# Kernel tuning notes

Measured on AMD Instinct MI355X. Metric: run time of the kernel, lower is better.

## Reference

```python
import jax, jax.numpy as jnp
import numpy as np

NEG_POS_RATIO = 3
BETA = 1.0
ALPHA = 2.0


def _smooth_ex_loss(pred, tgt):
    # a = beta / (1 - exp(-alpha)); c = a - beta - beta/alpha
    a = BETA / (1.0 - np.exp(-ALPHA))
    c = a - BETA - BETA / ALPHA
    diff = jnp.abs(pred - tgt)
    return jnp.where(diff < 1.0,
                     a * (diff + (jnp.exp(-ALPHA * diff) - 1.0) / ALPHA),
                     BETA * diff + c)


def setup_inputs() -> dict:
    key = jax.random.key(0)
    k1, k2, k3, k4 = jax.random.split(key, 4)
    B, P, C = 128, 8732, 21
    return {
        "confidence": jax.random.normal(k1, (B, P, C), dtype=jnp.float32),
        "predicted_locations": jax.random.normal(k2, (B, P, 4), dtype=jnp.float32),
        "labels": jax.random.randint(k3, (B, P), 0, C, dtype=jnp.int64),
        "gt_locations": jax.random.normal(k4, (B, P, 4), dtype=jnp.float32),
    }


def reference(confidence, predicted_locations, labels, gt_locations):
    # confidence: [B, P, C]; labels: [B, P]; locations: [B, P, 4]
    logp = jax.nn.log_softmax(confidence, axis=2)
    pos_mask = labels > 0

    # --- hard negative mining (no-grad in original) ---
    bg_loss = jax.lax.stop_gradient(-logp[:, :, 0])          # [B, P]
    num_pos = pos_mask.sum(axis=1, keepdims=True)             # [B, 1]
    num_neg = num_pos * NEG_POS_RATIO
    mined = jnp.where(pos_mask, -jnp.inf, bg_loss)
    idx = jnp.argsort(-mined, axis=1)                         # descending sort
    orders = jnp.argsort(idx, axis=1)                         # rank of each prior
    neg_mask = orders < num_neg
    mask = pos_mask | neg_mask                                # [B, P]

    # --- classification loss: sum of CE over mined priors ---
    per_elem_ce = -jnp.take_along_axis(logp, labels[..., None], axis=2)[..., 0]
    classification_loss = jnp.sum(jnp.where(mask, per_elem_ce, 0.0))

    # --- localization loss: smooth-ex loss over positive priors ---
    loc = _smooth_ex_loss(predicted_locations, gt_locations)  # [B, P, 4]
    smooth_sum = jnp.sum(jnp.where(pos_mask[..., None], loc, 0.0))

    n_pos_total = pos_mask.sum().astype(jnp.float32)
    return (smooth_sum / n_pos_total, classification_loss / n_pos_total)
```

## Files before the change

### kernel.cpp

```cpp
#include <hip/hip_runtime.h>
#include <cstdint>


#define B_ 128
#define P_ 8732
#define C_ 21
constexpr int TPB = 128;
constexpr int SPR = 28;
constexpr int SPAN = 312;
constexpr int NCHK = 5;
constexpr int GRID = B_ * SPR / 2;
constexpr int SLOTS = SPR / 2;
constexpr int CHB = 64 * C_ * 4;

typedef const __attribute__((address_space(1))) uint32_t* gas_u32p;
typedef __attribute__((address_space(3))) uint32_t* las_u32p;

__device__ __forceinline__ float waveSumF(float v) {
#pragma unroll
  for (int o = 32; o; o >>= 1) v += __shfl_down(v, o);
  return v;
}
__device__ __forceinline__ int waveSumI(int v) {
#pragma unroll
  for (int o = 32; o; o >>= 1) v += __shfl_down(v, o);
  return v;
}
__device__ __forceinline__ double waveSumD(double v) {
#pragma unroll
  for (int o = 32; o; o >>= 1) v += __shfl_down(v, o);
  return v;
}

__device__ __forceinline__ void stage(const char* g, float* l, int bytes, int lane) {
#pragma unroll
  for (int j = 0; j < 6; ++j) {
    const int off = (j << 10) + (lane << 4);
    if (off < bytes)
      __builtin_amdgcn_global_load_lds((gas_u32p)(g + off),
                                       (las_u32p)(l + (j << 8)), 16, 0, 0);
  }
}

#define SMEX(d) (((d) < 1.f) ? (1.1565176427496657f * ((d) + (__expf(-2.f * (d)) - 1.f) * 0.5f)) \
                             : ((d) - 0.3434823572503343f))

__device__ __forceinline__ void prior21(const float* lp, int lab, float4 pr, float4 gv,
                                        bool act, float& sm, float& cp, float& cn, int& np) {
  const float f0 = lp[0], f1 = lp[1], f2 = lp[2], f3 = lp[3], f4 = lp[4];
  const float f5 = lp[5], f6 = lp[6], f7 = lp[7], f8 = lp[8], f9 = lp[9];
  const float f10 = lp[10], f11 = lp[11], f12 = lp[12], f13 = lp[13], f14 = lp[14];
  const float f15 = lp[15], f16 = lp[16], f17 = lp[17], f18 = lp[18], f19 = lp[19];
  const float f20 = lp[20];
  float m = fmaxf(fmaxf(fmaxf(fmaxf(f0, f1), fmaxf(f2, f3)),
                        fmaxf(fmaxf(f4, f5), fmaxf(f6, f7))),
                  fmaxf(fmaxf(fmaxf(f8, f9), fmaxf(f10, f11)),
                        fmaxf(fmaxf(f12, f13), fmaxf(f14, f15))));
  m = fmaxf(m, fmaxf(fmaxf(fmaxf(f16, f17), fmaxf(f18, f19)), f20));
  float s = __expf(f0 - m) + __expf(f1 - m) + __expf(f2 - m) + __expf(f3 - m);
  s += __expf(f4 - m) + __expf(f5 - m) + __expf(f6 - m) + __expf(f7 - m);
  s += __expf(f8 - m) + __expf(f9 - m) + __expf(f10 - m) + __expf(f11 - m);
  s += __expf(f12 - m) + __expf(f13 - m) + __expf(f14 - m) + __expf(f15 - m);
  s += __expf(f16 - m) + __expf(f17 - m) + __expf(f18 - m) + __expf(f19 - m);
  s += __expf(f20 - m);
  float xl = f0;
  xl = (lab == 1) ? f1 : xl;   xl = (lab == 2) ? f2 : xl;
  xl = (lab == 3) ? f3 : xl;   xl = (lab == 4) ? f4 : xl;
  xl = (lab == 5) ? f5 : xl;   xl = (lab == 6) ? f6 : xl;
  xl = (lab == 7) ? f7 : xl;   xl = (lab == 8) ? f8 : xl;
  xl = (lab == 9) ? f9 : xl;   xl = (lab == 10) ? f10 : xl;
  xl = (lab == 11) ? f11 : xl; xl = (lab == 12) ? f12 : xl;
  xl = (lab == 13) ? f13 : xl; xl = (lab == 14) ? f14 : xl;
  xl = (lab == 15) ? f15 : xl; xl = (lab == 16) ? f16 : xl;
  xl = (lab == 17) ? f17 : xl; xl = (lab == 18) ? f18 : xl;
  xl = (lab == 19) ? f19 : xl; xl = (lab == 20) ? f20 : xl;
  const float ce = m + __logf(s) - xl;

  float d, smx;
  d = fabsf(pr.x - gv.x); smx = SMEX(d);
  d = fabsf(pr.y - gv.y); smx += SMEX(d);
  d = fabsf(pr.z - gv.z); smx += SMEX(d);
  d = fabsf(pr.w - gv.w); smx += SMEX(d);

  const bool pos = act && (lab > 0);
  sm += pos ? smx : 0.f;
  cp += pos ? ce : 0.f;
  cn += (act && lab == 0) ? ce : 0.f;
  np += pos ? 1 : 0;
}

__global__ __launch_bounds__(TPB, 3) void k_main(
    const float* __restrict__ conf, const float* __restrict__ pred,
    const int* __restrict__ labels, const float* __restrict__ gt,
    float4* __restrict__ part) {
  __shared__ __align__(16) float sbuf[2][2][64 * C_];
  __shared__ float redf[6];
  __shared__ int redi[2];
  const int tid = threadIdx.x;
  const int wid = tid >> 6, lane = tid & 63;
  const int row = blockIdx.x / SLOTS;
  const int pair = blockIdx.x % SLOTS;
  const int s = pair * 2 + wid;
  const int ps = s * SPAN;
  const int spc = min(SPAN, P_ - ps);
  const size_t rp = (size_t)row * P_;
  const char* cbase = (const char*)conf + (rp + (size_t)ps) * (C_ * 4);
  const float4* pred4 = (const float4*)pred;
  const float4* gt4 = (const float4*)gt;
  float* wbuf0 = sbuf[wid][0];
  float* wbuf1 = sbuf[wid][1];

  stage(cbase, wbuf0, 64 * C_ * 4, lane);
  int labr;
  float4 prr, gvr;
  {
    const size_t gp = rp + ps + lane;
    labr = labels[gp];
    prr = pred4[gp];
    gvr = gt4[gp];
  }
  asm volatile("s_waitcnt vmcnt(0)" ::: "memory");
  __builtin_amdgcn_sched_barrier(0);

  float sm = 0.f, cp = 0.f, cn = 0.f;
  int np = 0;

#pragma unroll
  for (int k = 0; k < NCHK; ++k) {
    float* cbuf = (k & 1) ? wbuf1 : wbuf0;
    float* nbuf = (k & 1) ? wbuf0 : wbuf1;
    int labn = 0;
    float4 prn = make_float4(0, 0, 0, 0), gvn = prn;
    if (k + 1 < NCHK) {
      const int cntn = min(64, spc - ((k + 1) << 6));
      stage(cbase + (size_t)(k + 1) * CHB, nbuf, cntn * (C_ * 4), lane);
      int idx = ((k + 1) << 6) + lane;
      if (idx >= spc) idx = spc - 1;
      const size_t gp = rp + ps + idx;
      labn = labels[gp];
      prn = pred4[gp];
      gvn = gt4[gp];
    }

    const int cnt = min(64, spc - (k << 6));
    prior21(&cbuf[lane * C_], labr, prr, gvr, lane < cnt, sm, cp, cn, np);

    asm volatile("s_waitcnt vmcnt(0)" ::: "memory");
    __builtin_amdgcn_sched_barrier(0);
    labr = labn; prr = prn; gvr = gvn;
  }

  const float r0 = waveSumF(sm), r1 = waveSumF(cp), r2 = waveSumF(cn);
  const int r3 = waveSumI(np);
  if (lane == 0) { redf[wid] = r0; redf[2 + wid] = r1; redf[4 + wid] = r2; redi[wid] = r3; }
  __syncthreads();
  if (tid == 0) {
    part[blockIdx.x] = make_float4(redf[0] + redf[1], redf[2] + redf[3],
                                   redf[4] + redf[5], (float)(redi[0] + redi[1]));
  }
}

__device__ __forceinline__ unsigned keyCE(const float* __restrict__ conf,
                                          const int* __restrict__ labels,
                                          int b, int p, float& ce) {
  const float* row = conf + ((size_t)b * P_ + p) * C_;
  float m = row[0];
  for (int c = 1; c < C_; ++c) m = fmaxf(m, row[c]);
  float s = 0.f;
  for (int c = 0; c < C_; ++c) s += __expf(row[c] - m);
  const float lse = m + __logf(s);
  const int lab = labels[(size_t)b * P_ + p];
  ce = lse - row[lab];
  if (lab > 0) return 0u;
  unsigned u = __float_as_uint(lse - row[0]);
  u = (u & 0x80000000u) ? ~u : (u | 0x80000000u);
  return u ? u : 1u;
}

__global__ __launch_bounds__(128) void k_tail(
    const float4* __restrict__ part, const float* __restrict__ conf,
    const int* __restrict__ labels, float* __restrict__ out) {
  const int tid = threadIdx.x;
  const int wid = tid >> 6, lane = tid & 63;
  __shared__ int s_np[B_], s_flag[B_];
  __shared__ double sdA[2], sdB[2], sdC[2];
  __shared__ int siN[2];
  __shared__ double s_extra;
  __shared__ int icnt[2];
  __shared__ float fsum[2];

  double sm = 0.0, cp = 0.0, cnSel = 0.0;
  int npr = 0;
  {
    double cn = 0.0;
#pragma unroll
    for (int i = 0; i < SLOTS; ++i) {
      const float4 v = part[tid * SLOTS + i];
      sm += (double)v.x;
      cp += (double)v.y;
      cn += (double)v.z;
      npr += (int)v.w;
    }
    s_np[tid] = npr;
    const int fl = (3 * npr < P_ - npr) ? 1 : 0;
    s_flag[tid] = fl;
    if (!fl) cnSel = cn;
  }
  const double t1 = waveSumD(sm), t2 = waveSumD(cp), t3 = waveSumD(cnSel);
  const int t4 = waveSumI(npr);
  if (lane == 0) { sdA[wid] = t1; sdB[wid] = t2; sdC[wid] = t3; siN[wid] = t4; }
  if (tid == 0) s_extra = 0.0;
  __syncthreads();

  for (int b = 0; b < B_; ++b) {
    if (!s_flag[b]) continue;
    const int need = 3 * s_np[b];
    unsigned long long lo = 1, hi = 0xFFFFFFFFull, ans = 1;
    while (lo <= hi) {
      const unsigned long long mid = lo + ((hi - lo) >> 1);
      int c = 0;
      float dummy;
      for (int p = tid; p < P_; p += 128)
        if ((unsigned long long)keyCE(conf, labels, b, p, dummy) >= mid) c++;
      c = waveSumI(c);
      if (lane == 0) icnt[wid] = c;
      __syncthreads();
      const int tot = icnt[0] + icnt[1];
      if (tot >= need) { ans = mid; lo = mid + 1; } else { hi = mid - 1; }
      __syncthreads();
    }
    int cgt = 0;
    float sgt = 0.f;
    for (int p = tid; p < P_; p += 128) {
      float ce;
      const unsigned long long k = keyCE(conf, labels, b, p, ce);
      if (k > ans) { cgt++; sgt += ce; }
    }
    cgt = waveSumI(cgt);
    sgt = waveSumF(sgt);
    if (lane == 0) { icnt[wid] = cgt; fsum[wid] = sgt; }
    __syncthreads();
    if (tid == 0) {
      const int gtot = icnt[0] + icnt[1];
      double sx = (double)(fsum[0] + fsum[1]);
      int rm = need - gtot;
      int taken = 0;
      for (int p = 0; p < P_ && taken < rm; ++p) {
        float ce;
        if (keyCE(conf, labels, b, p, ce) == ans) { sx += ce; taken++; }
      }
      s_extra += sx;
    }
    __syncthreads();
  }

  if (tid == 0) {
    const double G0 = sdA[0] + sdA[1];
    const double G1 = sdB[0] + sdB[1];
    const double G2 = sdC[0] + sdC[1] + s_extra;
    const double N = (double)(siN[0] + siN[1]);
    out[0] = (float)(G0 / N);
    out[1] = (float)((G1 + G2) / N);
  }
}

extern "C" void kernel_launch(void* const* d_in, const int* in_sizes, int n_in,
                              void* d_out, int out_size, void* d_ws, size_t ws_size,
                              hipStream_t stream) {
  const float* conf = (const float*)d_in[0];
  const float* pred = (const float*)d_in[1];
  const int* labels = (const int*)d_in[2];
  const float* gt = (const float*)d_in[3];
  float* out = (float*)d_out;

  float4* part = (float4*)d_ws;

  hipLaunchKernelGGL(k_main, dim3(GRID), dim3(TPB), 0, stream,
                     conf, pred, labels, gt, part);
  hipLaunchKernelGGL(k_tail, dim3(1), dim3(128), 0, stream,
                     part, conf, labels, out);
}
```

Baseline: 41.98 us.

## Use single-wave blocks with triple-buffered LDS ring and deeper prefetch

Replaces the two-wave blocks, each with its own double buffer, by one-wave blocks that own a 640-prior span and stream it through a three-slot LDS ring. Up to two chunks stay in flight, with partial vmcnt waits and per-chunk bounds clamping in place of byte-count guards. Block-level shared reduction is dropped because each block writes its partial directly. The goal is to hide global-load latency better and cut sync overhead, at the cost of fewer, longer-lived blocks and more LDS per wave.

```diff
diff --git a/kernel.cpp b/kernel.cpp
--- a/kernel.cpp
+++ b/kernel.cpp
@@ -5,13 +5,14 @@
 #define B_ 128
 #define P_ 8732
 #define C_ 21
-constexpr int TPB = 128;
-constexpr int SPR = 28;
-constexpr int SPAN = 312;
-constexpr int NCHK = 5;
-constexpr int GRID = B_ * SPR / 2;
-constexpr int SLOTS = SPR / 2;
+constexpr int TPB = 64;
+constexpr int SPR = 14;
+constexpr int SPAN = 640;
+constexpr int NCHK = 10;
+constexpr int GRID = B_ * SPR;
 constexpr int CHB = 64 * C_ * 4;
+constexpr int BUFF = 1536;
+constexpr size_t NE = (size_t)B_ * P_;
 
 typedef const __attribute__((address_space(1))) uint32_t* gas_u32p;
 typedef __attribute__((address_space(3))) uint32_t* las_u32p;
@@ -32,13 +33,13 @@
   return v;
 }
 
-__device__ __forceinline__ void stage(const char* g, float* l, int bytes, int lane) {
+__device__ __forceinline__ void stage6(const char* g, const char* gend,
+                                       float* l, int lane) {
 #pragma unroll
   for (int j = 0; j < 6; ++j) {
-    const int off = (j << 10) + (lane << 4);
-    if (off < bytes)
-      __builtin_amdgcn_global_load_lds((gas_u32p)(g + off),
-                                       (las_u32p)(l + (j << 8)), 16, 0, 0);
+    const char* s = g + (j << 10) + (lane << 4);
+    s = (s > gend) ? gend : s;
+    __builtin_amdgcn_global_load_lds((gas_u32p)s, (las_u32p)(l + (j << 8)), 16, 0, 0);
   }
 }
 
@@ -89,75 +90,64 @@
   np += pos ? 1 : 0;
 }
 
-__global__ __launch_bounds__(TPB, 3) void k_main(
+__global__ __launch_bounds__(TPB) void k_main(
     const float* __restrict__ conf, const float* __restrict__ pred,
     const int* __restrict__ labels, const float* __restrict__ gt,
     float4* __restrict__ part) {
-  __shared__ __align__(16) float sbuf[2][2][64 * C_];
-  __shared__ float redf[6];
-  __shared__ int redi[2];
-  const int tid = threadIdx.x;
-  const int wid = tid >> 6, lane = tid & 63;
-  const int row = blockIdx.x / SLOTS;
-  const int pair = blockIdx.x % SLOTS;
-  const int s = pair * 2 + wid;
+  __shared__ __align__(16) float ring[3][BUFF];
+  const int lane = threadIdx.x;
+  const int row = blockIdx.x / SPR;
+  const int s = blockIdx.x % SPR;
   const int ps = s * SPAN;
-  const int spc = min(SPAN, P_ - ps);
   const size_t rp = (size_t)row * P_;
   const char* cbase = (const char*)conf + (rp + (size_t)ps) * (C_ * 4);
+  const char* gend = (const char*)conf + NE * (C_ * 4) - 16;
   const float4* pred4 = (const float4*)pred;
   const float4* gt4 = (const float4*)gt;
-  float* wbuf0 = sbuf[wid][0];
-  float* wbuf1 = sbuf[wid][1];
-
-  stage(cbase, wbuf0, 64 * C_ * 4, lane);
-  int labr;
-  float4 prr, gvr;
-  {
-    const size_t gp = rp + ps + lane;
-    labr = labels[gp];
-    prr = pred4[gp];
-    gvr = gt4[gp];
-  }
-  asm volatile("s_waitcnt vmcnt(0)" ::: "memory");
-  __builtin_amdgcn_sched_barrier(0);
+
+  int labs[3];
+  float4 prs[3], gvs[3];
+
+#pragma unroll
+  for (int k = 0; k < 3; ++k) {
+    stage6(cbase + (size_t)k * CHB, gend, ring[k], lane);
+    size_t gp = rp + ps + (k << 6) + lane;
+    if (gp > NE - 1) gp = NE - 1;
+    labs[k] = labels[gp];
+    prs[k] = pred4[gp];
+    gvs[k] = gt4[gp];
+  }
 
   float sm = 0.f, cp = 0.f, cn = 0.f;
   int np = 0;
 
 #pragma unroll
   for (int k = 0; k < NCHK; ++k) {
-    float* cbuf = (k & 1) ? wbuf1 : wbuf0;
-    float* nbuf = (k & 1) ? wbuf0 : wbuf1;
-    int labn = 0;
-    float4 prn = make_float4(0, 0, 0, 0), gvn = prn;
-    if (k + 1 < NCHK) {
-      const int cntn = min(64, spc - ((k + 1) << 6));
-      stage(cbase + (size_t)(k + 1) * CHB, nbuf, cntn * (C_ * 4), lane);
-      int idx = ((k + 1) << 6) + lane;
-      if (idx >= spc) idx = spc - 1;
-      const size_t gp = rp + ps + idx;
-      labn = labels[gp];
-      prn = pred4[gp];
-      gvn = gt4[gp];
-    }
-
-    const int cnt = min(64, spc - (k << 6));
-    prior21(&cbuf[lane * C_], labr, prr, gvr, lane < cnt, sm, cp, cn, np);
-
-    asm volatile("s_waitcnt vmcnt(0)" ::: "memory");
+    if (k < 8)       asm volatile("s_waitcnt vmcnt(18)" ::: "memory");
+    else if (k == 8) asm volatile("s_waitcnt vmcnt(9)" ::: "memory");
+    else             asm volatile("s_waitcnt vmcnt(0)" ::: "memory");
     __builtin_amdgcn_sched_barrier(0);
-    labr = labn; prr = prn; gvr = gvn;
+
+    const bool act = (ps + (k << 6) + lane) < P_;
+    prior21(&ring[k % 3][lane * C_], labs[k % 3], prs[k % 3], gvs[k % 3],
+            act, sm, cp, cn, np);
+
+    if (k + 3 < NCHK) {
+      asm volatile("s_waitcnt lgkmcnt(0)" ::: "memory");
+      __builtin_amdgcn_sched_barrier(0);
+      stage6(cbase + (size_t)(k + 3) * CHB, gend, ring[k % 3], lane);
+      size_t gp = rp + ps + ((k + 3) << 6) + lane;
+      if (gp > NE - 1) gp = NE - 1;
+      labs[k % 3] = labels[gp];
+      prs[k % 3] = pred4[gp];
+      gvs[k % 3] = gt4[gp];
+    }
   }
 
   const float r0 = waveSumF(sm), r1 = waveSumF(cp), r2 = waveSumF(cn);
   const int r3 = waveSumI(np);
-  if (lane == 0) { redf[wid] = r0; redf[2 + wid] = r1; redf[4 + wid] = r2; redi[wid] = r3; }
-  __syncthreads();
-  if (tid == 0) {
-    part[blockIdx.x] = make_float4(redf[0] + redf[1], redf[2] + redf[3],
-                                   redf[4] + redf[5], (float)(redi[0] + redi[1]));
-  }
+  if (lane == 0)
+    part[blockIdx.x] = make_float4(r0, r1, r2, (float)r3);
 }
 
 __device__ __forceinline__ unsigned keyCE(const float* __restrict__ conf,
@@ -194,8 +184,8 @@
   {
     double cn = 0.0;
 #pragma unroll
-    for (int i = 0; i < SLOTS; ++i) {
-      const float4 v = part[tid * SLOTS + i];
+    for (int i = 0; i < SPR; ++i) {
+      const float4 v = part[tid * SPR + i];
       sm += (double)v.x;
       cp += (double)v.y;
       cn += (double)v.z;
```

Measured after the change: 45.45 us. 1.08x slower.
